# Kernel tuning notes

Hardware: AMD Instinct MI355X
Metric: run time of the kernel (lower is better)

## Reference

```python
import jax, jax.numpy as jnp
import numpy as np

N = 50000
E = 1600000
NFEAT = 128
NHID = 128
NEG_SLOPE_ATT = 0.2   # GATConv attention leaky_relu
NEG_SLOPE_ACT = 0.01  # F.leaky_relu default between layers


def setup_inputs() -> dict:
    key = jax.random.key(0)
    ks = jax.random.split(key, 12)
    x = jax.random.normal(ks[0], (N, NFEAT), dtype=jnp.float32)
    edge_index = jax.random.randint(ks[1], (2, E), 0, N, dtype=jnp.int64)
    s1 = 1.0 / np.sqrt(NFEAT)
    s2 = 1.0 / np.sqrt(NHID)
    return {
        "x": x,
        "edge_index": edge_index,
        "W1": jax.random.normal(ks[2], (NFEAT, NHID), dtype=jnp.float32) * s1,
        "att_src1": jax.random.normal(ks[3], (NHID,), dtype=jnp.float32) * s2,
        "att_dst1": jax.random.normal(ks[4], (NHID,), dtype=jnp.float32) * s2,
        "b1": jnp.zeros((NHID,), dtype=jnp.float32),
        "W2": jax.random.normal(ks[5], (NHID, NHID), dtype=jnp.float32) * s2,
        "att_src2": jax.random.normal(ks[6], (NHID,), dtype=jnp.float32) * s2,
        "att_dst2": jax.random.normal(ks[7], (NHID,), dtype=jnp.float32) * s2,
        "b2": jnp.zeros((NHID,), dtype=jnp.float32),
    }


def _gat_conv(x, src, dst, W, a_src, a_dst, b):
    # single-head GATConv (PyG defaults), self-loops already in src/dst
    h = x @ W                                  # [N, nhid]
    alpha_s = h @ a_src                        # [N]
    alpha_d = h @ a_dst                        # [N]
    e = jax.nn.leaky_relu(alpha_s[src] + alpha_d[dst], NEG_SLOPE_ATT)  # [E']
    # softmax over incoming edges per destination node
    m = jax.ops.segment_max(e, dst, num_segments=N)
    e = jnp.exp(e - m[dst])
    denom = jax.ops.segment_sum(e, dst, num_segments=N)
    alpha = e / (denom[dst] + 1e-16)
    out = jax.ops.segment_sum(h[src] * alpha[:, None], dst, num_segments=N)
    return out + b


def reference(x, edge_index, W1, att_src1, att_dst1, b1, W2, att_src2, att_dst2, b2):
    loops = jnp.arange(N, dtype=edge_index.dtype)
    src = jnp.concatenate([edge_index[0], loops])  # add_self_loops=True
    dst = jnp.concatenate([edge_index[1], loops])
    h = _gat_conv(x, src, dst, W1, att_src1, att_dst1, b1)
    h = jax.nn.leaky_relu(h, NEG_SLOPE_ACT)
    out = _gat_conv(h, src, dst, W2, att_src2, att_dst2, b2)
    return out
```

## Files before the change

### kernel.cpp

```cpp
#include <hip/hip_runtime.h>
#include <hip/hip_fp16.h>

constexpr int N  = 50000;
constexpr int E  = 1600000;
constexpr int NF = 128;
constexpr int BSH = 128;
constexpr int NB = (N + BSH - 1) / BSH;
constexpr int CAP = 8192;
constexpr int EPB  = 8192;
constexpr int NBLK = (E + EPB - 1) / EPB;
constexpr int PACKW_BLKS = (2 * NF * NF + 1023) / 1024;
constexpr int GEMM1_BLKS = (N + 127) / 128;
constexpr int SCAPW = 128;

typedef _Float16 half8 __attribute__((ext_vector_type(8)));
typedef float    f32x4 __attribute__((ext_vector_type(4)));

__global__ __launch_bounds__(1024) void k_scatter_packw(
    const int* __restrict__ ei, int* __restrict__ bcur, int* __restrict__ packed,
    const float* __restrict__ W1, const float* __restrict__ W2,
    __half* __restrict__ P1, __half* __restrict__ P2,
    const float* __restrict__ as2, const float* __restrict__ ad2,
    float* __restrict__ w2as, float* __restrict__ w2ad) {
    int t = threadIdx.x;
    if (blockIdx.x == NBLK + PACKW_BLKS) {
        if (t < NF) {
            float ps = 0.f, pd = 0.f;
            for (int j = 0; j < NF; ++j) {
                float w = W2[t * NF + j];
                ps = fmaf(w, as2[j], ps);
                pd = fmaf(w, ad2[j], pd);
            }
            w2as[t] = ps; w2ad[t] = pd;
        }
        return;
    }
    if (blockIdx.x >= NBLK) {
        int tid = (blockIdx.x - NBLK) * 1024 + t;
        if (tid >= 2 * NF * NF) return;
        int which = tid >> 14;
        int id = tid & (NF * NF - 1);
        int k = id >> 7, n = id & 127;
        const float* W = which ? W2 : W1;
        __half* P = which ? P2 : P1;
        int ks = k >> 5, r = k & 31, ct = n >> 4;
        int lane = ((r >> 3) << 4) | (n & 15);
        int j = r & 7;
        P[((ks * 8 + ct) * 64 + lane) * 8 + j] = __float2half_rn(W[k * NF + n]);
        return;
    }
    __shared__ int h[NB], lcur[NB], garr[NB];
    for (int i = t; i < NB; i += 1024) h[i] = 0;
    __syncthreads();
    int base = blockIdx.x * EPB;
    int pk[EPB / 1024];
    int bk[EPB / 1024];
#pragma unroll
    for (int k = 0; k < EPB / 1024; ++k) {
        int i = base + k * 1024 + t;
        if (i < E) {
            int s = ei[i], d = ei[E + i];
            bk[k] = d >> 7;
            pk[k] = s | ((d & (BSH - 1)) << 16);
            atomicAdd(&h[bk[k]], 1);
        } else bk[k] = -1;
    }
    __syncthreads();
    for (int i = t; i < NB; i += 1024) {
        lcur[i] = 0;
        garr[i] = i * CAP + (h[i] ? atomicAdd(&bcur[i], h[i]) : 0);
    }
    __syncthreads();
#pragma unroll
    for (int k = 0; k < EPB / 1024; ++k) {
        if (bk[k] >= 0) {
            int p = garr[bk[k]] + atomicAdd(&lcur[bk[k]], 1);
            packed[p] = pk[k];
        }
    }
}

template <typename AT>
__device__ __forceinline__ void gemm_rows16(
    const AT* __restrict__ A, const half8* __restrict__ BP,
    const float* __restrict__ asv, const float* __restrict__ adv,
    __half* __restrict__ H16, float* __restrict__ AS, float* __restrict__ AD,
    int base, int lane) {
    int row_a = base + (lane & 15);
    if (row_a >= N) row_a = N - 1;
    const AT* Arow = A + (size_t)row_a * NF;

    f32x4 acc[8] = {};
#pragma unroll
    for (int ks = 0; ks < 4; ++ks) {
        int eo = (ks * 4 + (lane >> 4)) * 8;
        half8 a;
        if constexpr (sizeof(AT) == 4) {
            float4 u = *(const float4*)(Arow + eo);
            float4 v = *(const float4*)(Arow + eo + 4);
            a[0] = (_Float16)u.x; a[1] = (_Float16)u.y; a[2] = (_Float16)u.z; a[3] = (_Float16)u.w;
            a[4] = (_Float16)v.x; a[5] = (_Float16)v.y; a[6] = (_Float16)v.z; a[7] = (_Float16)v.w;
        } else {
            a = ((const half8*)Arow)[ks * 4 + (lane >> 4)];
        }
#pragma unroll
        for (int ct = 0; ct < 8; ++ct) {
            half8 b = BP[(ks * 8 + ct) * 64 + lane];
            acc[ct] = __builtin_amdgcn_mfma_f32_16x16x32_f16(a, b, acc[ct], 0, 0, 0);
        }
    }

    int colb = lane & 15;
    int rowq = base + (lane >> 4) * 4;
    float ps[4] = {0.f, 0.f, 0.f, 0.f};
    float pd[4] = {0.f, 0.f, 0.f, 0.f};
#pragma unroll
    for (int ct = 0; ct < 8; ++ct) {
        int col = ct * 16 + colb;
        float av = asv[col], dv = adv[col];
#pragma unroll
        for (int r = 0; r < 4; ++r) {
            float hv = acc[ct][r];
            if (rowq + r < N) H16[(size_t)(rowq + r) * NF + col] = __float2half_rn(hv);
            ps[r] = fmaf(hv, av, ps[r]);
            pd[r] = fmaf(hv, dv, pd[r]);
        }
    }
#pragma unroll
    for (int r = 0; r < 4; ++r) {
#pragma unroll
        for (int o = 1; o <= 8; o <<= 1) {
            ps[r] += __shfl_xor(ps[r], o);
            pd[r] += __shfl_xor(pd[r], o);
        }
    }
    if (colb == 0) {
#pragma unroll
        for (int r = 0; r < 4; ++r) {
            if (rowq + r < N) { AS[rowq + r] = ps[r]; AD[rowq + r] = pd[r]; }
        }
    }
}

__global__ __launch_bounds__(512) void k_csr_gemm1(
    const int* __restrict__ packed, const int* __restrict__ bcur,
    int* __restrict__ offB, int* __restrict__ offE, unsigned short* __restrict__ srcs,
    const float* __restrict__ X, const __half* __restrict__ Wpk,
    const float* __restrict__ asv, const float* __restrict__ adv,
    __half* __restrict__ H16, float* __restrict__ AS, float* __restrict__ AD) {
    int t = threadIdx.x;
    if ((blockIdx.x & 1) == 0) {
        int blk = blockIdx.x >> 1;
        int wave = t >> 6, lane = t & 63;
        int base = blk * 128 + wave * 16;
        gemm_rows16<float>(X, (const half8*)Wpk, asv, adv, H16, AS, AD, base, lane);
        return;
    }
    int b = blockIdx.x >> 1;
    int s0 = b * CAP;
    int n = bcur[b];
    __shared__ int buf[CAP];
    __shared__ int h[BSH], bas[BSH], lcur[BSH];
    for (int i = t; i < n; i += 512) buf[i] = packed[s0 + i];
    if (t < BSH) { h[t] = 0; lcur[t] = 0; }
    __syncthreads();
    for (int i = t; i < n; i += 512)
        atomicAdd(&h[(buf[i] >> 16) & (BSH - 1)], 1);
    __syncthreads();
    if (t < 64) {
        int v0 = h[2 * t], v1 = h[2 * t + 1];
        int pair = v0 + v1, x = pair;
#pragma unroll
        for (int o = 1; o < 64; o <<= 1) {
            int y = __shfl_up(x, o);
            if (t >= o) x += y;
        }
        int e0 = s0 + x - pair;
        int e1 = e0 + v0;
        bas[2 * t] = e0; bas[2 * t + 1] = e1;
        int d = b * BSH + 2 * t;
        if (d < N)     { offB[d] = e0;     offE[d] = e1; }
        if (d + 1 < N) { offB[d + 1] = e1; offE[d + 1] = s0 + x; }
    }
    __syncthreads();
    for (int i = t; i < n; i += 512) {
        int p = buf[i];
        int dl = (p >> 16) & (BSH - 1);
        int pos = bas[dl] + atomicAdd(&lcur[dl], 1);
        srcs[pos] = (unsigned short)(p & 0xFFFF);
    }
}

__global__ __launch_bounds__(1024) void k_agg1_gemm2(
    const __half* __restrict__ H16in, const float* __restrict__ AS, const float* __restrict__ AD,
    const int* __restrict__ offB, const int* __restrict__ offE,
    const unsigned short* __restrict__ srcs,
    const float* __restrict__ b1, const __half* __restrict__ Wpk2,
    const float* __restrict__ w2as, const float* __restrict__ w2ad,
    __half* __restrict__ H16out, float* __restrict__ AS2, float* __restrict__ AD2) {
    int wave = threadIdx.x >> 6, lane = threadIdx.x & 63;
    int d = blockIdx.x * 16 + wave;

    __shared__ float ssv[16][SCAPW];
    __shared__ unsigned short ssrc[16][SCAPW];
    __shared__ __half Y[16][136];

    int beg = offB[d], deg = offE[d] - beg;
    float ad = AD[d];

    float ls = 0.f;
    for (int i = lane; i < deg; i += 64) {
        int s = srcs[beg + i];
        float sv = AS[s] + ad;
        sv = (sv > 0.f) ? sv : 0.2f * sv;
        float e = __expf(fminf(sv, 60.f));
        if (i < SCAPW) { ssv[wave][i] = e; ssrc[wave][i] = (unsigned short)s; }
        ls += e;
    }
#pragma unroll
    for (int o = 1; o <= 32; o <<= 1) ls += __shfl_xor(ls, o);
    float slv = AS[d] + ad;
    slv = (slv > 0.f) ? slv : 0.2f * slv;
    float es = __expf(fminf(slv, 60.f));
    ls += es;
    float inv = 1.f / (ls + 1e-16f);

    int tx = lane & 15, u = lane >> 4;
    float acc[8] = {0.f, 0.f, 0.f, 0.f, 0.f, 0.f, 0.f, 0.f};
    for (int j0 = 0; j0 < deg; j0 += 8) {
        int i0 = j0 + u, i1 = j0 + 4 + u;
        float e0 = 0.f, e1 = 0.f;
        int s0 = 0, s1 = 0;
        bool v0 = i0 < deg, v1 = i1 < deg;
        if (v0) {
            if (i0 < SCAPW) { e0 = ssv[wave][i0]; s0 = ssrc[wave][i0]; }
            else {
                s0 = srcs[beg + i0];
                float sv = AS[s0] + ad;
                sv = (sv > 0.f) ? sv : 0.2f * sv;
                e0 = __expf(fminf(sv, 60.f));
            }
        }
        if (v1) {
            if (i1 < SCAPW) { e1 = ssv[wave][i1]; s1 = ssrc[wave][i1]; }
            else {
                s1 = srcs[beg + i1];
                float sv = AS[s1] + ad;
                sv = (sv > 0.f) ? sv : 0.2f * sv;
                e1 = __expf(fminf(sv, 60.f));
            }
        }
        union { float4 f; __half2 h[4]; } va, vb;
        if (v0) va.f = *reinterpret_cast<const float4*>(H16in + (size_t)s0 * NF + tx * 8);
        if (v1) vb.f = *reinterpret_cast<const float4*>(H16in + (size_t)s1 * NF + tx * 8);
        if (v0) {
            float2 f0 = __half22float2(va.h[0]);
            float2 f1 = __half22float2(va.h[1]);
            float2 f2 = __half22float2(va.h[2]);
            float2 f3 = __half22float2(va.h[3]);
            acc[0] = fmaf(e0, f0.x, acc[0]); acc[1] = fmaf(e0, f0.y, acc[1]);
            acc[2] = fmaf(e0, f1.x, acc[2]); acc[3] = fmaf(e0, f1.y, acc[3]);
            acc[4] = fmaf(e0, f2.x, acc[4]); acc[5] = fmaf(e0, f2.y, acc[5]);
            acc[6] = fmaf(e0, f3.x, acc[6]); acc[7] = fmaf(e0, f3.y, acc[7]);
        }
        if (v1) {
            float2 f0 = __half22float2(vb.h[0]);
            float2 f1 = __half22float2(vb.h[1]);
            float2 f2 = __half22float2(vb.h[2]);
            float2 f3 = __half22float2(vb.h[3]);
            acc[0] = fmaf(e1, f0.x, acc[0]); acc[1] = fmaf(e1, f0.y, acc[1]);
            acc[2] = fmaf(e1, f1.x, acc[2]); acc[3] = fmaf(e1, f1.y, acc[3]);
            acc[4] = fmaf(e1, f2.x, acc[4]); acc[5] = fmaf(e1, f2.y, acc[5]);
            acc[6] = fmaf(e1, f3.x, acc[6]); acc[7] = fmaf(e1, f3.y, acc[7]);
        }
    }
#pragma unroll
    for (int o = 16; o <= 32; o <<= 1) {
#pragma unroll
        for (int i = 0; i < 8; ++i) acc[i] += __shfl_xor(acc[i], o);
    }
    {
        union { float4 f; __half2 h[4]; } vs;
        vs.f = *reinterpret_cast<const float4*>(H16in + (size_t)d * NF + tx * 8);
        float2 f0 = __half22float2(vs.h[0]);
        float2 f1 = __half22float2(vs.h[1]);
        float2 f2 = __half22float2(vs.h[2]);
        float2 f3 = __half22float2(vs.h[3]);
        acc[0] = fmaf(es, f0.x, acc[0]); acc[1] = fmaf(es, f0.y, acc[1]);
        acc[2] = fmaf(es, f1.x, acc[2]); acc[3] = fmaf(es, f1.y, acc[3]);
        acc[4] = fmaf(es, f2.x, acc[4]); acc[5] = fmaf(es, f2.y, acc[5]);
        acc[6] = fmaf(es, f3.x, acc[6]); acc[7] = fmaf(es, f3.y, acc[7]);
    }
    float y[8];
    float ps = 0.f, pd = 0.f;
#pragma unroll
    for (int i = 0; i < 8; ++i) {
        float v = acc[i] * inv + b1[tx * 8 + i];
        v = (v < 0.f) ? 0.01f * v : v;
        y[i] = v;
        ps = fmaf(v, w2as[tx * 8 + i], ps);
        pd = fmaf(v, w2ad[tx * 8 + i], pd);
    }
#pragma unroll
    for (int o = 1; o <= 8; o <<= 1) { ps += __shfl_xor(ps, o); pd += __shfl_xor(pd, o); }
    if (lane == 0) { AS2[d] = ps; AD2[d] = pd; }
    if (lane < 16) {
        half8 hv;
#pragma unroll
        for (int i = 0; i < 8; ++i) hv[i] = (_Float16)y[i];
        *(half8*)(&Y[wave][tx * 8]) = hv;
    }
    __syncthreads();
    if (wave < 8) {
        const half8* BP = (const half8*)Wpk2;
        f32x4 c4 = {};
#pragma unroll
        for (int ks = 0; ks < 4; ++ks) {
            half8 a = *(const half8*)(&Y[lane & 15][ks * 32 + (lane >> 4) * 8]);
            half8 b = BP[(ks * 8 + wave) * 64 + lane];
            c4 = __builtin_amdgcn_mfma_f32_16x16x32_f16(a, b, c4, 0, 0, 0);
        }
        int base = blockIdx.x * 16;
        int colb = lane & 15;
        int rowq = (lane >> 4) * 4;
#pragma unroll
        for (int r = 0; r < 4; ++r)
            H16out[(size_t)(base + rowq + r) * NF + wave * 16 + colb] = __float2half_rn(c4[r]);
    }
}

__global__ __launch_bounds__(256) void k_aggregate2(
    const __half* __restrict__ H16, const float* __restrict__ AS, const float* __restrict__ AD,
    const int* __restrict__ offB, const int* __restrict__ offE,
    const unsigned short* __restrict__ srcs,
    const float* __restrict__ bias, float* __restrict__ OUT) {
    int wave = threadIdx.x >> 6, lane = threadIdx.x & 63;
    int d = blockIdx.x * 4 + wave;

    __shared__ float ssv[4][SCAPW];
    __shared__ unsigned short ssrc[4][SCAPW];

    int beg = offB[d], deg = offE[d] - beg;
    float ad = AD[d];

    float ls = 0.f;
    for (int i = lane; i < deg; i += 64) {
        int s = srcs[beg + i];
        float sv = AS[s] + ad;
        sv = (sv > 0.f) ? sv : 0.2f * sv;
        float e = __expf(fminf(sv, 60.f));
        if (i < SCAPW) { ssv[wave][i] = e; ssrc[wave][i] = (unsigned short)s; }
        ls += e;
    }
#pragma unroll
    for (int o = 1; o <= 32; o <<= 1) ls += __shfl_xor(ls, o);
    float slv = AS[d] + ad;
    slv = (slv > 0.f) ? slv : 0.2f * slv;
    float es = __expf(fminf(slv, 60.f));
    ls += es;
    float inv = 1.f / (ls + 1e-16f);

    int tx = lane & 15, u = lane >> 4;
    float acc[8] = {0.f, 0.f, 0.f, 0.f, 0.f, 0.f, 0.f, 0.f};
    for (int j0 = 0; j0 < deg; j0 += 8) {
        int i0 = j0 + u, i1 = j0 + 4 + u;
        float e0 = 0.f, e1 = 0.f;
        int s0 = 0, s1 = 0;
        bool v0 = i0 < deg, v1 = i1 < deg;
        if (v0) {
            if (i0 < SCAPW) { e0 = ssv[wave][i0]; s0 = ssrc[wave][i0]; }
            else {
                s0 = srcs[beg + i0];
                float sv = AS[s0] + ad;
                sv = (sv > 0.f) ? sv : 0.2f * sv;
                e0 = __expf(fminf(sv, 60.f));
            }
        }
        if (v1) {
            if (i1 < SCAPW) { e1 = ssv[wave][i1]; s1 = ssrc[wave][i1]; }
            else {
                s1 = srcs[beg + i1];
                float sv = AS[s1] + ad;
                sv = (sv > 0.f) ? sv : 0.2f * sv;
                e1 = __expf(fminf(sv, 60.f));
            }
        }
        union { float4 f; __half2 h[4]; } va, vb;
        if (v0) va.f = *reinterpret_cast<const float4*>(H16 + (size_t)s0 * NF + tx * 8);
        if (v1) vb.f = *reinterpret_cast<const float4*>(H16 + (size_t)s1 * NF + tx * 8);
        if (v0) {
            float2 f0 = __half22float2(va.h[0]);
            float2 f1 = __half22float2(va.h[1]);
            float2 f2 = __half22float2(va.h[2]);
            float2 f3 = __half22float2(va.h[3]);
            acc[0] = fmaf(e0, f0.x, acc[0]); acc[1] = fmaf(e0, f0.y, acc[1]);
            acc[2] = fmaf(e0, f1.x, acc[2]); acc[3] = fmaf(e0, f1.y, acc[3]);
            acc[4] = fmaf(e0, f2.x, acc[4]); acc[5] = fmaf(e0, f2.y, acc[5]);
            acc[6] = fmaf(e0, f3.x, acc[6]); acc[7] = fmaf(e0, f3.y, acc[7]);
        }
        if (v1) {
            float2 f0 = __half22float2(vb.h[0]);
            float2 f1 = __half22float2(vb.h[1]);
            float2 f2 = __half22float2(vb.h[2]);
            float2 f3 = __half22float2(vb.h[3]);
            acc[0] = fmaf(e1, f0.x, acc[0]); acc[1] = fmaf(e1, f0.y, acc[1]);
            acc[2] = fmaf(e1, f1.x, acc[2]); acc[3] = fmaf(e1, f1.y, acc[3]);
            acc[4] = fmaf(e1, f2.x, acc[4]); acc[5] = fmaf(e1, f2.y, acc[5]);
            acc[6] = fmaf(e1, f3.x, acc[6]); acc[7] = fmaf(e1, f3.y, acc[7]);
        }
    }
#pragma unroll
    for (int o = 16; o <= 32; o <<= 1) {
#pragma unroll
        for (int i = 0; i < 8; ++i) acc[i] += __shfl_xor(acc[i], o);
    }
    {
        union { float4 f; __half2 h[4]; } vs;
        vs.f = *reinterpret_cast<const float4*>(H16 + (size_t)d * NF + tx * 8);
        float2 f0 = __half22float2(vs.h[0]);
        float2 f1 = __half22float2(vs.h[1]);
        float2 f2 = __half22float2(vs.h[2]);
        float2 f3 = __half22float2(vs.h[3]);
        acc[0] = fmaf(es, f0.x, acc[0]); acc[1] = fmaf(es, f0.y, acc[1]);
        acc[2] = fmaf(es, f1.x, acc[2]); acc[3] = fmaf(es, f1.y, acc[3]);
        acc[4] = fmaf(es, f2.x, acc[4]); acc[5] = fmaf(es, f2.y, acc[5]);
        acc[6] = fmaf(es, f3.x, acc[6]); acc[7] = fmaf(es, f3.y, acc[7]);
    }
    if (lane < 16) {
        float o8[8];
#pragma unroll
        for (int i = 0; i < 8; ++i) o8[i] = acc[i] * inv + bias[tx * 8 + i];
        float4 w0 = {o8[0], o8[1], o8[2], o8[3]};
        float4 w1 = {o8[4], o8[5], o8[6], o8[7]};
        ((float4*)OUT)[(size_t)d * 32 + tx * 2]     = w0;
        ((float4*)OUT)[(size_t)d * 32 + tx * 2 + 1] = w1;
    }
}

extern "C" void kernel_launch(void* const* d_in, const int* in_sizes, int n_in,
                              void* d_out, int out_size, void* d_ws, size_t ws_size,
                              hipStream_t stream) {
    const float* x   = (const float*)d_in[0];
    const int*   ei  = (const int*)d_in[1];
    const float* W1  = (const float*)d_in[2];
    const float* as1 = (const float*)d_in[3];
    const float* ad1 = (const float*)d_in[4];
    const float* b1  = (const float*)d_in[5];
    const float* W2  = (const float*)d_in[6];
    const float* as2 = (const float*)d_in[7];
    const float* ad2 = (const float*)d_in[8];
    const float* b2  = (const float*)d_in[9];
    float* out = (float*)d_out;

    char* p = (char*)d_ws;
    auto alloc = [&](size_t bytes) { char* r = p; p += (bytes + 255) & ~size_t(255); return (void*)r; };
    int* bcur  = (int*)alloc(sizeof(int) * NB);
    int* offB  = (int*)alloc(sizeof(int) * N);
    int* offE  = (int*)alloc(sizeof(int) * N);
    unsigned short* srcs = (unsigned short*)alloc(sizeof(unsigned short) * (size_t)NB * CAP);
    __half* H16a  = (__half*)alloc(sizeof(__half) * (size_t)N * NF);
    __half* H16b  = (__half*)alloc(sizeof(__half) * (size_t)N * NF);
    __half* Wpk1  = (__half*)alloc(sizeof(__half) * NF * NF);
    __half* Wpk2  = (__half*)alloc(sizeof(__half) * NF * NF);
    float* AS1 = (float*)alloc(sizeof(float) * N);
    float* AD1 = (float*)alloc(sizeof(float) * N);
    float* AS2 = (float*)alloc(sizeof(float) * N);
    float* AD2 = (float*)alloc(sizeof(float) * N);
    float* w2as = (float*)alloc(sizeof(float) * NF);
    float* w2ad = (float*)alloc(sizeof(float) * NF);
    int* packed = (int*)alloc(sizeof(int) * (size_t)NB * CAP);

    hipMemsetAsync(bcur, 0, sizeof(int) * NB, stream);
    k_scatter_packw<<<NBLK + PACKW_BLKS + 1, 1024, 0, stream>>>(
        ei, bcur, packed, W1, W2, Wpk1, Wpk2, as2, ad2, w2as, w2ad);
    k_csr_gemm1<<<2 * GEMM1_BLKS, 512, 0, stream>>>(packed, bcur, offB, offE, srcs,
                                                    x, Wpk1, as1, ad1, H16a, AS1, AD1);
    k_agg1_gemm2<<<N / 16, 1024, 0, stream>>>(H16a, AS1, AD1, offB, offE, srcs,
                                              b1, Wpk2, w2as, w2ad, H16b, AS2, AD2);
    k_aggregate2<<<N / 4, 256, 0, stream>>>(H16b, AS2, AD2, offB, offE, srcs, b2, out);
}
```

Measured before the change: 173.1 us.

## Sort destination nodes by in-degree to balance aggregation waves

Builds a per-node in-degree histogram during CSR construction, then a new kernel counting-sorts node ids by degree into a permutation. Both aggregation kernels then process destinations in permuted order, so waves in a block get similar degrees and wait less on the slowest wave. This adds a kernel launch, atomics and an extra level of indirection, and the output rows and H16 rows are written scattered instead of contiguously. With uniformly random edges the degree spread is narrow, so there may be little imbalance to remove.

Measured after the change: 423.2 us. +144.5%, slower.

```diff
diff --git a/kernel.cpp b/kernel.cpp
--- a/kernel.cpp
+++ b/kernel.cpp
@@ -12,6 +12,7 @@
 constexpr int PACKW_BLKS = (2 * NF * NF + 1023) / 1024;
 constexpr int GEMM1_BLKS = (N + 127) / 128;
 constexpr int SCAPW = 128;
+constexpr int DBINS = 256;
 
 typedef _Float16 half8 __attribute__((ext_vector_type(8)));
 typedef float    f32x4 __attribute__((ext_vector_type(4)));
@@ -145,6 +146,7 @@
 __global__ __launch_bounds__(512) void k_csr_gemm1(
     const int* __restrict__ packed, const int* __restrict__ bcur,
     int* __restrict__ offB, int* __restrict__ offE, unsigned short* __restrict__ srcs,
+    int* __restrict__ deg, int* __restrict__ dhist,
     const float* __restrict__ X, const __half* __restrict__ Wpk,
     const float* __restrict__ asv, const float* __restrict__ adv,
     __half* __restrict__ H16, float* __restrict__ AS, float* __restrict__ AD) {
@@ -167,6 +169,14 @@
     for (int i = t; i < n; i += 512)
         atomicAdd(&h[(buf[i] >> 16) & (BSH - 1)], 1);
     __syncthreads();
+    if (t < BSH) {
+        int d = b * BSH + t;
+        if (d < N) {
+            deg[d] = h[t];
+            int bin = h[t] < DBINS - 1 ? h[t] : DBINS - 1;
+            atomicAdd(&dhist[bin], 1);
+        }
+    }
     if (t < 64) {
         int v0 = h[2 * t], v1 = h[2 * t + 1];
         int pair = v0 + v1, x = pair;
@@ -191,19 +201,44 @@
     }
 }
 
+__global__ __launch_bounds__(256) void k_permscatter(
+    const int* __restrict__ deg, const int* __restrict__ dhist,
+    int* __restrict__ dcnt, int* __restrict__ perm) {
+    __shared__ int sc[DBINS];
+    int t = threadIdx.x;
+    int v = dhist[t];
+    sc[t] = v;
+    __syncthreads();
+    for (int o = 1; o < DBINS; o <<= 1) {
+        int a = (t >= o) ? sc[t - o] : 0;
+        __syncthreads();
+        sc[t] += a;
+        __syncthreads();
+    }
+    int d = blockIdx.x * 256 + t;
+    if (d >= N) return;
+    int dg = deg[d];
+    int bin = dg < DBINS - 1 ? dg : DBINS - 1;
+    int base = sc[bin] - dhist[bin];
+    int pos = base + atomicAdd(&dcnt[bin], 1);
+    perm[pos] = d;
+}
+
 __global__ __launch_bounds__(1024) void k_agg1_gemm2(
     const __half* __restrict__ H16in, const float* __restrict__ AS, const float* __restrict__ AD,
     const int* __restrict__ offB, const int* __restrict__ offE,
-    const unsigned short* __restrict__ srcs,
+    const unsigned short* __restrict__ srcs, const int* __restrict__ perm,
     const float* __restrict__ b1, const __half* __restrict__ Wpk2,
     const float* __restrict__ w2as, const float* __restrict__ w2ad,
     __half* __restrict__ H16out, float* __restrict__ AS2, float* __restrict__ AD2) {
     int wave = threadIdx.x >> 6, lane = threadIdx.x & 63;
-    int d = blockIdx.x * 16 + wave;
+    int d = perm[blockIdx.x * 16 + wave];
 
     __shared__ float ssv[16][SCAPW];
     __shared__ unsigned short ssrc[16][SCAPW];
     __shared__ __half Y[16][136];
+    __shared__ int dd[16];
+    if (lane == 0) dd[wave] = d;
 
     int beg = offB[d], deg = offE[d] - beg;
     float ad = AD[d];
@@ -320,22 +355,21 @@
             half8 b = BP[(ks * 8 + wave) * 64 + lane];
             c4 = __builtin_amdgcn_mfma_f32_16x16x32_f16(a, b, c4, 0, 0, 0);
         }
-        int base = blockIdx.x * 16;
         int colb = lane & 15;
         int rowq = (lane >> 4) * 4;
 #pragma unroll
         for (int r = 0; r < 4; ++r)
-            H16out[(size_t)(base + rowq + r) * NF + wave * 16 + colb] = __float2half_rn(c4[r]);
+            H16out[(size_t)dd[rowq + r] * NF + wave * 16 + colb] = __float2half_rn(c4[r]);
     }
 }
 
 __global__ __launch_bounds__(256) void k_aggregate2(
     const __half* __restrict__ H16, const float* __restrict__ AS, const float* __restrict__ AD,
     const int* __restrict__ offB, const int* __restrict__ offE,
-    const unsigned short* __restrict__ srcs,
+    const unsigned short* __restrict__ srcs, const int* __restrict__ perm,
     const float* __restrict__ bias, float* __restrict__ OUT) {
     int wave = threadIdx.x >> 6, lane = threadIdx.x & 63;
-    int d = blockIdx.x * 4 + wave;
+    int d = perm[blockIdx.x * 4 + wave];
 
     __shared__ float ssv[4][SCAPW];
     __shared__ unsigned short ssrc[4][SCAPW];
@@ -454,9 +488,14 @@
 
     char* p = (char*)d_ws;
     auto alloc = [&](size_t bytes) { char* r = p; p += (bytes + 255) & ~size_t(255); return (void*)r; };
-    int* bcur  = (int*)alloc(sizeof(int) * NB);
+    int* zreg  = (int*)alloc(sizeof(int) * (NB + 2 * DBINS));
+    int* bcur  = zreg;
+    int* dhist = zreg + NB;
+    int* dcnt  = zreg + NB + DBINS;
     int* offB  = (int*)alloc(sizeof(int) * N);
     int* offE  = (int*)alloc(sizeof(int) * N);
+    int* deg   = (int*)alloc(sizeof(int) * N);
+    int* perm  = (int*)alloc(sizeof(int) * N);
     unsigned short* srcs = (unsigned short*)alloc(sizeof(unsigned short) * (size_t)NB * CAP);
     __half* H16a  = (__half*)alloc(sizeof(__half) * (size_t)N * NF);
     __half* H16b  = (__half*)alloc(sizeof(__half) * (size_t)N * NF);
@@ -470,12 +509,14 @@
     float* w2ad = (float*)alloc(sizeof(float) * NF);
     int* packed = (int*)alloc(sizeof(int) * (size_t)NB * CAP);
 
-    hipMemsetAsync(bcur, 0, sizeof(int) * NB, stream);
+    hipMemsetAsync(zreg, 0, sizeof(int) * (NB + 2 * DBINS), stream);
     k_scatter_packw<<<NBLK + PACKW_BLKS + 1, 1024, 0, stream>>>(
         ei, bcur, packed, W1, W2, Wpk1, Wpk2, as2, ad2, w2as, w2ad);
     k_csr_gemm1<<<2 * GEMM1_BLKS, 512, 0, stream>>>(packed, bcur, offB, offE, srcs,
+                                                    deg, dhist,
                                                     x, Wpk1, as1, ad1, H16a, AS1, AD1);
-    k_agg1_gemm2<<<N / 16, 1024, 0, stream>>>(H16a, AS1, AD1, offB, offE, srcs,
+    k_permscatter<<<(N + 255) / 256, 256, 0, stream>>>(deg, dhist, dcnt, perm);
+    k_agg1_gemm2<<<N / 16, 1024, 0, stream>>>(H16a, AS1, AD1, offB, offE, srcs, perm,
                                               b1, Wpk2, w2as, w2ad, H16b, AS2, AD2);
-    k_aggregate2<<<N / 4, 256, 0, stream>>>(H16b, AS2, AD2, offB, offE, srcs, b2, out);
-}
+    k_aggregate2<<<N / 4, 256, 0, stream>>>(H16b, AS2, AD2, offB, offE, srcs, perm, b2, out);
+}
```

## Sort destination nodes by in-degree within buckets to balance wave work

Applied to the files above, without the earlier changes.

Computes a per-bucket permutation of destination nodes ordered by in-degree during CSR construction, then has both aggregation kernels process nodes in that order. Waves within a block then handle nodes of similar degree, which is meant to reduce divergence and idle waves waiting on high-degree neighbours. In exchange it adds an O(BSH^2) rank computation per bucket and an extra indirection, and it scatters GEMM2 output rows, which loses write coalescing.

Measured after the change: 191.3 us, median of 3. 10.5% more time.

```diff
diff --git a/kernel.cpp b/kernel.cpp
--- a/kernel.cpp
+++ b/kernel.cpp
@@ -145,6 +145,7 @@
 __global__ __launch_bounds__(512) void k_csr_gemm1(
     const int* __restrict__ packed, const int* __restrict__ bcur,
     int* __restrict__ offB, int* __restrict__ offE, unsigned short* __restrict__ srcs,
+    int* __restrict__ perm,
     const float* __restrict__ X, const __half* __restrict__ Wpk,
     const float* __restrict__ asv, const float* __restrict__ adv,
     __half* __restrict__ H16, float* __restrict__ AS, float* __restrict__ AD) {
@@ -167,6 +168,20 @@
     for (int i = t; i < n; i += 512)
         atomicAdd(&h[(buf[i] >> 16) & (BSH - 1)], 1);
     __syncthreads();
+    if (t < BSH) {
+        int d = b * BSH + t;
+        if (d < N) {
+            int mydeg = h[t];
+            int rank = 0;
+            for (int j = 0; j < BSH; ++j) {
+                if (b * BSH + j < N) {
+                    int hj = h[j];
+                    rank += (hj < mydeg) || (hj == mydeg && j < t);
+                }
+            }
+            perm[b * BSH + rank] = d;
+        }
+    }
     if (t < 64) {
         int v0 = h[2 * t], v1 = h[2 * t + 1];
         int pair = v0 + v1, x = pair;
@@ -194,16 +209,18 @@
 __global__ __launch_bounds__(1024) void k_agg1_gemm2(
     const __half* __restrict__ H16in, const float* __restrict__ AS, const float* __restrict__ AD,
     const int* __restrict__ offB, const int* __restrict__ offE,
-    const unsigned short* __restrict__ srcs,
+    const unsigned short* __restrict__ srcs, const int* __restrict__ perm,
     const float* __restrict__ b1, const __half* __restrict__ Wpk2,
     const float* __restrict__ w2as, const float* __restrict__ w2ad,
     __half* __restrict__ H16out, float* __restrict__ AS2, float* __restrict__ AD2) {
     int wave = threadIdx.x >> 6, lane = threadIdx.x & 63;
-    int d = blockIdx.x * 16 + wave;
+    int d = perm[blockIdx.x * 16 + wave];
 
     __shared__ float ssv[16][SCAPW];
     __shared__ unsigned short ssrc[16][SCAPW];
     __shared__ __half Y[16][136];
+    __shared__ int dd[16];
+    if (lane == 0) dd[wave] = d;
 
     int beg = offB[d], deg = offE[d] - beg;
     float ad = AD[d];
@@ -320,22 +337,21 @@
             half8 b = BP[(ks * 8 + wave) * 64 + lane];
             c4 = __builtin_amdgcn_mfma_f32_16x16x32_f16(a, b, c4, 0, 0, 0);
         }
-        int base = blockIdx.x * 16;
         int colb = lane & 15;
         int rowq = (lane >> 4) * 4;
 #pragma unroll
         for (int r = 0; r < 4; ++r)
-            H16out[(size_t)(base + rowq + r) * NF + wave * 16 + colb] = __float2half_rn(c4[r]);
+            H16out[(size_t)dd[rowq + r] * NF + wave * 16 + colb] = __float2half_rn(c4[r]);
     }
 }
 
 __global__ __launch_bounds__(256) void k_aggregate2(
     const __half* __restrict__ H16, const float* __restrict__ AS, const float* __restrict__ AD,
     const int* __restrict__ offB, const int* __restrict__ offE,
-    const unsigned short* __restrict__ srcs,
+    const unsigned short* __restrict__ srcs, const int* __restrict__ perm,
     const float* __restrict__ bias, float* __restrict__ OUT) {
     int wave = threadIdx.x >> 6, lane = threadIdx.x & 63;
-    int d = blockIdx.x * 4 + wave;
+    int d = perm[blockIdx.x * 4 + wave];
 
     __shared__ float ssv[4][SCAPW];
     __shared__ unsigned short ssrc[4][SCAPW];
@@ -457,6 +473,7 @@
     int* bcur  = (int*)alloc(sizeof(int) * NB);
     int* offB  = (int*)alloc(sizeof(int) * N);
     int* offE  = (int*)alloc(sizeof(int) * N);
+    int* perm  = (int*)alloc(sizeof(int) * N);
     unsigned short* srcs = (unsigned short*)alloc(sizeof(unsigned short) * (size_t)NB * CAP);
     __half* H16a  = (__half*)alloc(sizeof(__half) * (size_t)N * NF);
     __half* H16b  = (__half*)alloc(sizeof(__half) * (size_t)N * NF);
@@ -473,9 +490,9 @@
     hipMemsetAsync(bcur, 0, sizeof(int) * NB, stream);
     k_scatter_packw<<<NBLK + PACKW_BLKS + 1, 1024, 0, stream>>>(
         ei, bcur, packed, W1, W2, Wpk1, Wpk2, as2, ad2, w2as, w2ad);
-    k_csr_gemm1<<<2 * GEMM1_BLKS, 512, 0, stream>>>(packed, bcur, offB, offE, srcs,
+    k_csr_gemm1<<<2 * GEMM1_BLKS, 512, 0, stream>>>(packed, bcur, offB, offE, srcs, perm,
                                                     x, Wpk1, as1, ad1, H16a, AS1, AD1);
-    k_agg1_gemm2<<<N / 16, 1024, 0, stream>>>(H16a, AS1, AD1, offB, offE, srcs,
+    k_agg1_gemm2<<<N / 16, 1024, 0, stream>>>(H16a, AS1, AD1, offB, offE, srcs, perm,
                                               b1, Wpk2, w2as, w2ad, H16b, AS2, AD2);
-    k_aggregate2<<<N / 4, 256, 0, stream>>>(H16b, AS2, AD2, offB, offE, srcs, b2, out);
-}
+    k_aggregate2<<<N / 4, 256, 0, stream>>>(H16b, AS2, AD2, offB, offE, srcs, perm, b2, out);
+}
```
